# Optimization experiments

Hardware: AMD Instinct MI355X
Metric: run time of the kernel (lower is better)

## Reference

```python
import jax, jax.numpy as jnp
import numpy as np

N, C, IN, OUT = 32768, 8, 512, 512


def setup_inputs() -> dict:
    key = jax.random.key(0)
    k1, k2 = jax.random.split(key)
    x = jax.random.normal(k1, (N, C, IN), dtype=jnp.float32)
    # per-channel Linear weights, init std = in_features**-0.5 (as in torch module)
    W = jax.random.normal(k2, (C, OUT, IN), dtype=jnp.float32) * (IN ** -0.5)
    b = jnp.zeros((C, OUT), dtype=jnp.float32)
    return {"x": x, "W": W, "b": b}


def reference(x, W, b):
    # Fused per-channel linear: out[n,c,o] = sum_i x[n,c,i] * W[c,o,i] + b[c,o]
    # Replaces the Python loop over num_channels nn.Linear calls with one
    # batched GEMM over the channel dim.
    return jnp.einsum('nci,coi->nco', x, W) + b[None, :, :]
```

## Files before the change

### kernel.cpp

```cpp
#include <hip/hip_runtime.h>
#include <stdint.h>

#define N_TOT 32768
#define C_CH  8
#define K_IN  512
#define OUT_F 512

#define BM 128
#define BN 128
#define BK 64
#define NSTEPS (K_IN / BK)
#define LDA 72

typedef __attribute__((ext_vector_type(4))) float    f32x4;
typedef __attribute__((ext_vector_type(8))) short    s16x8;
typedef __attribute__((ext_vector_type(4))) uint32_t u32x4;

__device__ __forceinline__ void cvt_store8(short* dst, u32x4 v) {
  uint32_t r0 = v.x + 0x8000u;
  uint32_t r1 = v.y + 0x8000u;
  uint32_t r2 = v.z + 0x8000u;
  uint32_t r3 = v.w + 0x8000u;
  uint32_t p0 = __builtin_amdgcn_perm(r1, r0, 0x07060302u);
  uint32_t p1 = __builtin_amdgcn_perm(r3, r2, 0x07060302u);
  uint2 pk; pk.x = p0; pk.y = p1;
  *(uint2*)dst = pk;
}

extern "C" __global__ void __launch_bounds__(256, 2)
mcl_gemm(const float* __restrict__ xg, const float* __restrict__ wg,
         const float* __restrict__ bg, float* __restrict__ og) {
  __shared__ short lA[BM * LDA];
  __shared__ short lB[BN * LDA];

  const int bid   = blockIdx.x;
  const int c     = bid & 7;
  const int otile = (bid >> 3) & 3;
  const int ntile = bid >> 5;

  const int tid  = threadIdx.x;
  const int lane = tid & 63;
  const int wave = tid >> 6;
  const int wm   = wave & 1;
  const int wn   = wave >> 1;

  const int row0 = ntile * BM;
  const int col0 = otile * BN;

  const int sr  = tid >> 4;
  const int scf = (tid & 15) * 4;
  const float* ap = xg + ((size_t)(row0 + sr) * C_CH + c) * K_IN + scf;
  const float* bp = wg + ((size_t)c * OUT_F + (col0 + sr)) * K_IN + scf;
  short* aw = lA + sr * LDA + scf;
  short* bw = lB + sr * LDA + scf;

  const size_t a_row_stride = (size_t)16 * C_CH * K_IN;
  const size_t b_row_stride = (size_t)16 * K_IN;

  u32x4 areg[8], breg[8];
#pragma unroll
  for (int i = 0; i < 8; ++i) areg[i] = *(const u32x4*)(ap + (size_t)i * a_row_stride);
#pragma unroll
  for (int i = 0; i < 8; ++i) breg[i] = *(const u32x4*)(bp + (size_t)i * b_row_stride);

  f32x4 acc[4][4];
#pragma unroll
  for (int mi = 0; mi < 4; ++mi)
#pragma unroll
    for (int ni = 0; ni < 4; ++ni)
#pragma unroll
      for (int e = 0; e < 4; ++e) acc[mi][ni][e] = 0.0f;

  const int fl   = lane & 15;
  const int quad = lane >> 4;
  const short* arp = lA + (wm * 64 + fl) * LDA + quad * 8;
  const short* brp = lB + (wn * 64 + fl) * LDA + quad * 8;

  for (int step = 0; step < NSTEPS; ++step) {
#pragma unroll
    for (int i = 0; i < 8; ++i) cvt_store8(aw + i * 16 * LDA, areg[i]);
#pragma unroll
    for (int i = 0; i < 8; ++i) cvt_store8(bw + i * 16 * LDA, breg[i]);
    __syncthreads();

    if (step + 1 < NSTEPS) {
      const float* ap2 = ap + (step + 1) * BK;
      const float* bp2 = bp + (step + 1) * BK;
#pragma unroll
      for (int i = 0; i < 8; ++i) areg[i] = *(const u32x4*)(ap2 + (size_t)i * a_row_stride);
#pragma unroll
      for (int i = 0; i < 8; ++i) breg[i] = *(const u32x4*)(bp2 + (size_t)i * b_row_stride);
    }

#pragma unroll
    for (int kk = 0; kk < BK; kk += 32) {
      s16x8 af[4], bf[4];
#pragma unroll
      for (int mi = 0; mi < 4; ++mi)
        af[mi] = *(const s16x8*)(arp + mi * 16 * LDA + kk);
#pragma unroll
      for (int ni = 0; ni < 4; ++ni)
        bf[ni] = *(const s16x8*)(brp + ni * 16 * LDA + kk);
#pragma unroll
      for (int mi = 0; mi < 4; ++mi)
#pragma unroll
        for (int ni = 0; ni < 4; ++ni)
          acc[mi][ni] = __builtin_amdgcn_mfma_f32_16x16x32_bf16(af[mi], bf[ni], acc[mi][ni], 0, 0, 0);
    }
    __syncthreads();
  }

  float bias[4];
#pragma unroll
  for (int ni = 0; ni < 4; ++ni)
    bias[ni] = bg[c * OUT_F + col0 + wn * 64 + ni * 16 + fl];

#pragma unroll
  for (int mi = 0; mi < 4; ++mi) {
#pragma unroll
    for (int r = 0; r < 4; ++r) {
      const int n = row0 + wm * 64 + mi * 16 + quad * 4 + r;
      float* orow = og + ((size_t)n * C_CH + c) * OUT_F + col0 + wn * 64 + fl;
#pragma unroll
      for (int ni = 0; ni < 4; ++ni)
        __builtin_nontemporal_store(acc[mi][ni][r] + bias[ni], orow + ni * 16);
    }
  }
}

extern "C" void kernel_launch(void* const* d_in, const int* in_sizes, int n_in,
                              void* d_out, int out_size, void* d_ws, size_t ws_size,
                              hipStream_t stream) {
  const float* x = (const float*)d_in[0];
  const float* W = (const float*)d_in[1];
  const float* b = (const float*)d_in[2];
  float* out = (float*)d_out;
  dim3 grid((N_TOT / BM) * (OUT_F / BN) * C_CH);
  mcl_gemm<<<grid, dim3(256), 0, stream>>>(x, W, b, out);
}
```

Measured before the change: 918.5 us.

## Replace LDS-tiled GEMM with register-direct MFMA loads and pre-converted bf16 weights

Removes the shared-memory staging and barriers. Each wave now loads its x and W fragments straight from global memory into MFMA operand layout, using 32-row by 512-column blocks per channel. The fp32 weights are converted to bf16 once per call in a separate kernel into workspace, with a fallback that converts on the fly, and conversion uses the hardware pack instruction. Every block covers the full output width, so x is read only once. The trade-off is that weight fragments are re-read from L2 by every block with uncoalesced strided access, and there is less data reuse per loaded element.

```diff
diff --git a/kernel.cpp b/kernel.cpp
--- a/kernel.cpp
+++ b/kernel.cpp
@@ -5,127 +5,131 @@
 #define C_CH  8
 #define K_IN  512
 #define OUT_F 512
+#define NKS   (K_IN / 32)
+#define WB_ELEMS ((size_t)C_CH * OUT_F * K_IN)
 
-#define BM 128
-#define BN 128
-#define BK 64
-#define NSTEPS (K_IN / BK)
-#define LDA 72
+typedef __attribute__((ext_vector_type(4))) float f32x4;
+typedef __attribute__((ext_vector_type(8))) short s16x8;
 
-typedef __attribute__((ext_vector_type(4))) float    f32x4;
-typedef __attribute__((ext_vector_type(8))) short    s16x8;
-typedef __attribute__((ext_vector_type(4))) uint32_t u32x4;
+__device__ __forceinline__ s16x8 cvt_bf16x8(f32x4 lo, f32x4 hi) {
+  uint32_t p0, p1, p2, p3;
+  asm("v_cvt_pk_bf16_f32 %0, %1, %2" : "=v"(p0) : "v"(lo.x), "v"(lo.y));
+  asm("v_cvt_pk_bf16_f32 %0, %1, %2" : "=v"(p1) : "v"(lo.z), "v"(lo.w));
+  asm("v_cvt_pk_bf16_f32 %0, %1, %2" : "=v"(p2) : "v"(hi.x), "v"(hi.y));
+  asm("v_cvt_pk_bf16_f32 %0, %1, %2" : "=v"(p3) : "v"(hi.z), "v"(hi.w));
+  union { uint32_t u[4]; s16x8 v; } r;
+  r.u[0] = p0; r.u[1] = p1; r.u[2] = p2; r.u[3] = p3;
+  return r.v;
+}
 
-__device__ __forceinline__ void cvt_store8(short* dst, u32x4 v) {
-  uint32_t r0 = v.x + 0x8000u;
-  uint32_t r1 = v.y + 0x8000u;
-  uint32_t r2 = v.z + 0x8000u;
-  uint32_t r3 = v.w + 0x8000u;
-  uint32_t p0 = __builtin_amdgcn_perm(r1, r0, 0x07060302u);
-  uint32_t p1 = __builtin_amdgcn_perm(r3, r2, 0x07060302u);
-  uint2 pk; pk.x = p0; pk.y = p1;
-  *(uint2*)dst = pk;
+extern "C" __global__ void __launch_bounds__(256, 4)
+wconv(const float* __restrict__ w, unsigned short* __restrict__ wb) {
+  const size_t i = ((size_t)blockIdx.x * 256 + threadIdx.x) * 8;
+  f32x4 lo = *(const f32x4*)(w + i);
+  f32x4 hi = *(const f32x4*)(w + i + 4);
+  *(s16x8*)(wb + i) = cvt_bf16x8(lo, hi);
+}
+
+template <bool PRE>
+__device__ __forceinline__ void gemm_body(const float* __restrict__ xg,
+                                          const void* __restrict__ wsrc,
+                                          const float* __restrict__ bg,
+                                          float* __restrict__ og) {
+  const int bid  = blockIdx.x;
+  const int c    = bid & 7;
+  const int n0   = (bid >> 3) * 32;
+  const int tid  = (int)threadIdx.x;
+  const int lane = tid & 63;
+  const int wv   = tid >> 6;
+  const int o0   = wv * 128;
+  const int fl   = lane & 15;
+  const int quad = lane >> 4;
+
+  const float* ax0 = xg + ((size_t)(n0 + fl) * C_CH + c) * K_IN + quad * 8;
+  const float* ax1 = ax0 + (size_t)16 * C_CH * K_IN;
+
+  const unsigned short* bx[8];
+  const float* bxf[8];
+#pragma unroll
+  for (int ni = 0; ni < 8; ++ni) {
+    const size_t off = ((size_t)c * OUT_F + o0 + ni * 16 + fl) * K_IN + quad * 8;
+    bx[ni]  = (const unsigned short*)wsrc + off;
+    bxf[ni] = (const float*)wsrc + off;
+  }
+
+  f32x4 acc[2][8];
+#pragma unroll
+  for (int mi = 0; mi < 2; ++mi)
+#pragma unroll
+    for (int ni = 0; ni < 8; ++ni)
+#pragma unroll
+      for (int e = 0; e < 4; ++e) acc[mi][ni][e] = 0.0f;
+
+  f32x4 al0 = *(const f32x4*)(ax0);
+  f32x4 ah0 = *(const f32x4*)(ax0 + 4);
+  f32x4 al1 = *(const f32x4*)(ax1);
+  f32x4 ah1 = *(const f32x4*)(ax1 + 4);
+
+#pragma unroll
+  for (int ks = 0; ks < NKS; ++ks) {
+    s16x8 bf[8];
+    if constexpr (PRE) {
+#pragma unroll
+      for (int ni = 0; ni < 8; ++ni)
+        bf[ni] = *(const s16x8*)(bx[ni] + ks * 32);
+    } else {
+#pragma unroll
+      for (int ni = 0; ni < 8; ++ni) {
+        f32x4 blo = *(const f32x4*)(bxf[ni] + ks * 32);
+        f32x4 bhi = *(const f32x4*)(bxf[ni] + ks * 32 + 4);
+        bf[ni] = cvt_bf16x8(blo, bhi);
+      }
+    }
+    f32x4 nl0, nh0, nl1, nh1;
+    if (ks + 1 < NKS) {
+      nl0 = *(const f32x4*)(ax0 + (ks + 1) * 32);
+      nh0 = *(const f32x4*)(ax0 + (ks + 1) * 32 + 4);
+      nl1 = *(const f32x4*)(ax1 + (ks + 1) * 32);
+      nh1 = *(const f32x4*)(ax1 + (ks + 1) * 32 + 4);
+    }
+    const s16x8 af0 = cvt_bf16x8(al0, ah0);
+    const s16x8 af1 = cvt_bf16x8(al1, ah1);
+#pragma unroll
+    for (int ni = 0; ni < 8; ++ni) {
+      acc[0][ni] = __builtin_amdgcn_mfma_f32_16x16x32_bf16(af0, bf[ni], acc[0][ni], 0, 0, 0);
+      acc[1][ni] = __builtin_amdgcn_mfma_f32_16x16x32_bf16(af1, bf[ni], acc[1][ni], 0, 0, 0);
+    }
+    if (ks + 1 < NKS) { al0 = nl0; ah0 = nh0; al1 = nl1; ah1 = nh1; }
+  }
+
+  float bias[8];
+#pragma unroll
+  for (int ni = 0; ni < 8; ++ni)
+    bias[ni] = bg[c * OUT_F + o0 + ni * 16 + fl];
+
+#pragma unroll
+  for (int mi = 0; mi < 2; ++mi) {
+#pragma unroll
+    for (int r = 0; r < 4; ++r) {
+      const size_t n = (size_t)n0 + mi * 16 + quad * 4 + r;
+      float* orow = og + (n * C_CH + c) * OUT_F + o0 + fl;
+#pragma unroll
+      for (int ni = 0; ni < 8; ++ni)
+        __builtin_nontemporal_store(acc[mi][ni][r] + bias[ni], orow + ni * 16);
+    }
+  }
 }
 
 extern "C" __global__ void __launch_bounds__(256, 2)
-mcl_gemm(const float* __restrict__ xg, const float* __restrict__ wg,
-         const float* __restrict__ bg, float* __restrict__ og) {
-  __shared__ short lA[BM * LDA];
-  __shared__ short lB[BN * LDA];
+mcl_gemm_pre(const float* __restrict__ xg, const unsigned short* __restrict__ wb,
+             const float* __restrict__ bg, float* __restrict__ og) {
+  gemm_body<true>(xg, wb, bg, og);
+}
 
-  const int bid   = blockIdx.x;
-  const int c     = bid & 7;
-  const int otile = (bid >> 3) & 3;
-  const int ntile = bid >> 5;
-
-  const int tid  = threadIdx.x;
-  const int lane = tid & 63;
-  const int wave = tid >> 6;
-  const int wm   = wave & 1;
-  const int wn   = wave >> 1;
-
-  const int row0 = ntile * BM;
-  const int col0 = otile * BN;
-
-  const int sr  = tid >> 4;
-  const int scf = (tid & 15) * 4;
-  const float* ap = xg + ((size_t)(row0 + sr) * C_CH + c) * K_IN + scf;
-  const float* bp = wg + ((size_t)c * OUT_F + (col0 + sr)) * K_IN + scf;
-  short* aw = lA + sr * LDA + scf;
-  short* bw = lB + sr * LDA + scf;
-
-  const size_t a_row_stride = (size_t)16 * C_CH * K_IN;
-  const size_t b_row_stride = (size_t)16 * K_IN;
-
-  u32x4 areg[8], breg[8];
-#pragma unroll
-  for (int i = 0; i < 8; ++i) areg[i] = *(const u32x4*)(ap + (size_t)i * a_row_stride);
-#pragma unroll
-  for (int i = 0; i < 8; ++i) breg[i] = *(const u32x4*)(bp + (size_t)i * b_row_stride);
-
-  f32x4 acc[4][4];
-#pragma unroll
-  for (int mi = 0; mi < 4; ++mi)
-#pragma unroll
-    for (int ni = 0; ni < 4; ++ni)
-#pragma unroll
-      for (int e = 0; e < 4; ++e) acc[mi][ni][e] = 0.0f;
-
-  const int fl   = lane & 15;
-  const int quad = lane >> 4;
-  const short* arp = lA + (wm * 64 + fl) * LDA + quad * 8;
-  const short* brp = lB + (wn * 64 + fl) * LDA + quad * 8;
-
-  for (int step = 0; step < NSTEPS; ++step) {
-#pragma unroll
-    for (int i = 0; i < 8; ++i) cvt_store8(aw + i * 16 * LDA, areg[i]);
-#pragma unroll
-    for (int i = 0; i < 8; ++i) cvt_store8(bw + i * 16 * LDA, breg[i]);
-    __syncthreads();
-
-    if (step + 1 < NSTEPS) {
-      const float* ap2 = ap + (step + 1) * BK;
-      const float* bp2 = bp + (step + 1) * BK;
-#pragma unroll
-      for (int i = 0; i < 8; ++i) areg[i] = *(const u32x4*)(ap2 + (size_t)i * a_row_stride);
-#pragma unroll
-      for (int i = 0; i < 8; ++i) breg[i] = *(const u32x4*)(bp2 + (size_t)i * b_row_stride);
-    }
-
-#pragma unroll
-    for (int kk = 0; kk < BK; kk += 32) {
-      s16x8 af[4], bf[4];
-#pragma unroll
-      for (int mi = 0; mi < 4; ++mi)
-        af[mi] = *(const s16x8*)(arp + mi * 16 * LDA + kk);
-#pragma unroll
-      for (int ni = 0; ni < 4; ++ni)
-        bf[ni] = *(const s16x8*)(brp + ni * 16 * LDA + kk);
-#pragma unroll
-      for (int mi = 0; mi < 4; ++mi)
-#pragma unroll
-        for (int ni = 0; ni < 4; ++ni)
-          acc[mi][ni] = __builtin_amdgcn_mfma_f32_16x16x32_bf16(af[mi], bf[ni], acc[mi][ni], 0, 0, 0);
-    }
-    __syncthreads();
-  }
-
-  float bias[4];
-#pragma unroll
-  for (int ni = 0; ni < 4; ++ni)
-    bias[ni] = bg[c * OUT_F + col0 + wn * 64 + ni * 16 + fl];
-
-#pragma unroll
-  for (int mi = 0; mi < 4; ++mi) {
-#pragma unroll
-    for (int r = 0; r < 4; ++r) {
-      const int n = row0 + wm * 64 + mi * 16 + quad * 4 + r;
-      float* orow = og + ((size_t)n * C_CH + c) * OUT_F + col0 + wn * 64 + fl;
-#pragma unroll
-      for (int ni = 0; ni < 4; ++ni)
-        __builtin_nontemporal_store(acc[mi][ni][r] + bias[ni], orow + ni * 16);
-    }
-  }
+extern "C" __global__ void __launch_bounds__(256, 2)
+mcl_gemm_f32(const float* __restrict__ xg, const float* __restrict__ wg,
+             const float* __restrict__ bg, float* __restrict__ og) {
+  gemm_body<false>(xg, wg, bg, og);
 }
 
 extern "C" void kernel_launch(void* const* d_in, const int* in_sizes, int n_in,
@@ -135,6 +139,13 @@
   const float* W = (const float*)d_in[1];
   const float* b = (const float*)d_in[2];
   float* out = (float*)d_out;
-  dim3 grid((N_TOT / BM) * (OUT_F / BN) * C_CH);
-  mcl_gemm<<<grid, dim3(256), 0, stream>>>(x, W, b, out);
+
+  dim3 grid(C_CH * (N_TOT / 32));
+  if (d_ws && ws_size >= WB_ELEMS * sizeof(unsigned short)) {
+    unsigned short* wb = (unsigned short*)d_ws;
+    wconv<<<dim3((unsigned)(WB_ELEMS / (256 * 8))), dim3(256), 0, stream>>>(W, wb);
+    mcl_gemm_pre<<<grid, dim3(256), 0, stream>>>(x, wb, b, out);
+  } else {
+    mcl_gemm_f32<<<grid, dim3(256), 0, stream>>>(x, W, b, out);
+  }
 }
```

Result: slower. 1.467 ms (+59.8%).
